# Performance work log

Hardware: AMD Instinct MI355X
Metric: run time of the kernel (lower is better)

## Reference

```python
import jax, jax.numpy as jnp
import numpy as np

V, E, H, L = 50257, 1024, 1024, 512


def setup_inputs() -> dict:
    key = jax.random.key(0)
    ks = jax.random.split(key, 12)
    s = 0.02
    return {
        'input': jax.random.randint(ks[0], (1,), 0, V),
        'hidden': jax.random.normal(ks[1], (1, 1, H), dtype=jnp.float32),
        'encoder_outputs': jax.random.normal(ks[2], (L, H), dtype=jnp.float32),
        'emb_table': jax.random.normal(ks[3], (V, E), dtype=jnp.float32) * s,
        'attn_W': jax.random.normal(ks[4], (L, E + H), dtype=jnp.float32) * s,
        'attn_b': jax.random.normal(ks[5], (L,), dtype=jnp.float32) * s,
        'W_ih': jax.random.normal(ks[6], (3 * H, E + H), dtype=jnp.float32) * s,
        'W_hh': jax.random.normal(ks[7], (3 * H, H), dtype=jnp.float32) * s,
        'b_ih': jax.random.normal(ks[8], (3 * H,), dtype=jnp.float32) * s,
        'b_hh': jax.random.normal(ks[9], (3 * H,), dtype=jnp.float32) * s,
        'out_W': jax.random.normal(ks[10], (V, H), dtype=jnp.float32) * s,
        'out_b': jax.random.normal(ks[11], (V,), dtype=jnp.float32) * s,
    }


def reference(input, hidden, encoder_outputs, emb_table, attn_W, attn_b,
              W_ih, W_hh, b_ih, b_hh, out_W, out_b):
    # Dropout is inference-identity here.
    embedded = emb_table[input].reshape(1, E)                      # [1, E]
    h = hidden[0]                                                  # [1, H]
    attn_in = jnp.concatenate([embedded, h], axis=1)               # [1, E+H]
    attn_weights = jax.nn.softmax(attn_in @ attn_W.T + attn_b, axis=1)  # [1, L]
    attn_applied = attn_weights @ encoder_outputs                  # [1, H]
    x = jnp.concatenate([embedded, attn_applied], axis=1)          # [1, E+H]
    # PyTorch GRU cell, gate order (r, z, n)
    gi = x @ W_ih.T + b_ih                                         # [1, 3H]
    gh = h @ W_hh.T + b_hh                                         # [1, 3H]
    i_r, i_z, i_n = gi[:, :H], gi[:, H:2 * H], gi[:, 2 * H:]
    h_r, h_z, h_n = gh[:, :H], gh[:, H:2 * H], gh[:, 2 * H:]
    r = jax.nn.sigmoid(i_r + h_r)
    z = jax.nn.sigmoid(i_z + h_z)
    n = jnp.tanh(i_n + r * h_n)
    h_new = (1.0 - z) * n + z * h                                  # [1, H]
    log_probs = jax.nn.log_softmax(h_new @ out_W.T + out_b, axis=1)  # [1, V]
    return log_probs, h_new[None], attn_weights
```

## Files before the change

kernel.cpp:

```cpp
#include <hip/hip_runtime.h>
#include <math.h>

#define V 50257
#define E 1024
#define H 1024
#define L 512

#define OUT_LP 0
#define OUT_H  50257
#define OUT_AW 51281

#define WS_S    0
#define WS_W    512
#define WS_X    1024
#define WS_GH   3072
#define WS_GI   6144
#define WS_HN   9216
#define WS_BMAX 10240
#define WS_SUM  12288
#define WS_MAX  12289

__global__ void k1_scores_gh(const int* __restrict__ input,
                             const float* __restrict__ hidden,
                             const float* __restrict__ emb_table,
                             const float* __restrict__ attn_W,
                             const float* __restrict__ attn_b,
                             const float* __restrict__ W_hh,
                             const float* __restrict__ b_hh,
                             float* __restrict__ ws) {
    int wave = (blockIdx.x * blockDim.x + threadIdx.x) >> 6;
    int lane = threadIdx.x & 63;
    const float4* h4 = (const float4*)hidden;
    if (wave < L) {
        int l = wave;
        const float4* emb4 = (const float4*)(emb_table + (size_t)input[0] * E);
        const float4* w4 = (const float4*)(attn_W + (size_t)l * (E + H));
        float acc = 0.f;
        for (int i = lane; i < (E + H) / 4; i += 64) {
            float4 a = (i < E / 4) ? emb4[i] : h4[i - E / 4];
            float4 b = w4[i];
            acc += a.x * b.x + a.y * b.y + a.z * b.z + a.w * b.w;
        }
        for (int off = 32; off > 0; off >>= 1) acc += __shfl_down(acc, off, 64);
        if (lane == 0) ws[WS_S + l] = acc + attn_b[l];
    } else {
        int k = wave - L;
        if (k < 3 * H) {
            const float4* w4 = (const float4*)(W_hh + (size_t)k * H);
            float acc = 0.f;
            for (int i = lane; i < H / 4; i += 64) {
                float4 a = h4[i];
                float4 b = w4[i];
                acc += a.x * b.x + a.y * b.y + a.z * b.z + a.w * b.w;
            }
            for (int off = 32; off > 0; off >>= 1) acc += __shfl_down(acc, off, 64);
            if (lane == 0) ws[WS_GH + k] = acc + b_hh[k];
        }
    }
}

__global__ void k2_softmax(const int* __restrict__ input,
                           const float* __restrict__ emb_table,
                           float* __restrict__ ws, float* __restrict__ out) {
    __shared__ float red[8];
    __shared__ float bmax, bsum;
    int t = threadIdx.x;
    int lane = t & 63, wid = t >> 6;
    float v = ws[WS_S + t];
    float m = v;
    for (int off = 32; off > 0; off >>= 1) m = fmaxf(m, __shfl_down(m, off, 64));
    if (lane == 0) red[wid] = m;
    __syncthreads();
    if (t == 0) {
        float mm = red[0];
        for (int i = 1; i < 8; i++) mm = fmaxf(mm, red[i]);
        bmax = mm;
    }
    __syncthreads();
    float e = expf(v - bmax);
    float s = e;
    for (int off = 32; off > 0; off >>= 1) s += __shfl_down(s, off, 64);
    if (lane == 0) red[wid] = s;
    __syncthreads();
    if (t == 0) {
        float ss = 0.f;
        for (int i = 0; i < 8; i++) ss += red[i];
        bsum = ss;
    }
    __syncthreads();
    float w = e / bsum;
    ws[WS_W + t] = w;
    out[OUT_AW + t] = w;
    const float* emb = emb_table + (size_t)input[0] * E;
    ws[WS_X + t] = emb[t];
    ws[WS_X + 512 + t] = emb[512 + t];
    ws[WS_X + E + t] = 0.f;
    ws[WS_X + E + 512 + t] = 0.f;
}

__global__ void k3_applied(const float* __restrict__ enc, float* __restrict__ ws) {
    int jc = blockIdx.x & 3, lc = blockIdx.x >> 2;
    int j = jc * 256 + threadIdx.x;
    int l0 = lc * 64;
    float acc = 0.f;
    for (int l = l0; l < l0 + 64; ++l)
        acc += ws[WS_W + l] * enc[(size_t)l * H + j];
    atomicAdd(&ws[WS_X + E + j], acc);
}

__global__ void k4_gi(const float* __restrict__ W_ih, const float* __restrict__ b_ih,
                      float* __restrict__ ws) {
    int wave = (blockIdx.x * blockDim.x + threadIdx.x) >> 6;
    int lane = threadIdx.x & 63;
    if (wave >= 3 * H) return;
    const float4* x4 = (const float4*)(ws + WS_X);
    const float4* w4 = (const float4*)(W_ih + (size_t)wave * (E + H));
    float acc = 0.f;
    for (int i = lane; i < (E + H) / 4; i += 64) {
        float4 a = x4[i];
        float4 b = w4[i];
        acc += a.x * b.x + a.y * b.y + a.z * b.z + a.w * b.w;
    }
    for (int off = 32; off > 0; off >>= 1) acc += __shfl_down(acc, off, 64);
    if (lane == 0) ws[WS_GI + wave] = acc + b_ih[wave];
}

__global__ void k5_combine(const float* __restrict__ hidden, float* __restrict__ ws,
                           float* __restrict__ out) {
    int k = blockIdx.x * 256 + threadIdx.x;
    float gir = ws[WS_GI + k],         ghr = ws[WS_GH + k];
    float giz = ws[WS_GI + H + k],     ghz = ws[WS_GH + H + k];
    float gin = ws[WS_GI + 2 * H + k], ghn = ws[WS_GH + 2 * H + k];
    float r = 1.f / (1.f + expf(-(gir + ghr)));
    float z = 1.f / (1.f + expf(-(giz + ghz)));
    float n = tanhf(gin + r * ghn);
    float hn = (1.f - z) * n + z * hidden[k];
    ws[WS_HN + k] = hn;
    out[OUT_H + k] = hn;
    if (k == 0) ws[WS_SUM] = 0.f;
}

__global__ void k6_logits(const float* __restrict__ out_W, const float* __restrict__ out_b,
                          float* __restrict__ ws, float* __restrict__ out) {
    __shared__ float hn[H];
    __shared__ float wmax[4];
    int t = threadIdx.x;
    for (int i = t; i < H; i += 256) hn[i] = ws[WS_HN + i];
    __syncthreads();
    int lane = t & 63, wid = t >> 6;
    int gwave = blockIdx.x * 4 + wid;
    float lmax = -INFINITY;
    const float4* h4 = (const float4*)hn;
    for (int row = gwave; row < V; row += 8192) {
        const float4* w4 = (const float4*)(out_W + (size_t)row * H);
        float acc = 0.f;
        for (int i = lane; i < H / 4; i += 64) {
            float4 a = h4[i];
            float4 b = w4[i];
            acc += a.x * b.x + a.y * b.y + a.z * b.z + a.w * b.w;
        }
        for (int off = 32; off > 0; off >>= 1) acc += __shfl_down(acc, off, 64);
        if (lane == 0) {
            float lg = acc + out_b[row];
            out[OUT_LP + row] = lg;
            lmax = fmaxf(lmax, lg);
        }
    }
    if (lane == 0) wmax[wid] = lmax;
    __syncthreads();
    if (t == 0) {
        float m = fmaxf(fmaxf(wmax[0], wmax[1]), fmaxf(wmax[2], wmax[3]));
        ws[WS_BMAX + blockIdx.x] = m;
    }
}

__global__ void k7_sumexp(float* __restrict__ ws, const float* __restrict__ out) {
    __shared__ float red[4];
    __shared__ float gmax;
    int t = threadIdx.x;
    int lane = t & 63, wid = t >> 6;
    float m = -INFINITY;
    for (int i = t; i < 2048; i += 256) m = fmaxf(m, ws[WS_BMAX + i]);
    for (int off = 32; off > 0; off >>= 1) m = fmaxf(m, __shfl_down(m, off, 64));
    if (lane == 0) red[wid] = m;
    __syncthreads();
    if (t == 0) gmax = fmaxf(fmaxf(red[0], red[1]), fmaxf(red[2], red[3]));
    __syncthreads();
    float M = gmax;
    float s = 0.f;
    for (int i = blockIdx.x * 256 + t; i < V; i += 64 * 256) s += expf(out[i] - M);
    for (int off = 32; off > 0; off >>= 1) s += __shfl_down(s, off, 64);
    if (lane == 0) red[wid] = s;
    __syncthreads();
    if (t == 0) {
        float bs = red[0] + red[1] + red[2] + red[3];
        atomicAdd(&ws[WS_SUM], bs);
        if (blockIdx.x == 0) ws[WS_MAX] = M;
    }
}

__global__ void k8_logprobs(const float* __restrict__ ws, float* __restrict__ out) {
    int i = blockIdx.x * 256 + threadIdx.x;
    if (i < V) out[i] = out[i] - ws[WS_MAX] - logf(ws[WS_SUM]);
}

extern "C" void kernel_launch(void* const* d_in, const int* in_sizes, int n_in,
                              void* d_out, int out_size, void* d_ws, size_t ws_size,
                              hipStream_t stream) {
    const int*   input   = (const int*)d_in[0];
    const float* hidden  = (const float*)d_in[1];
    const float* enc     = (const float*)d_in[2];
    const float* emb     = (const float*)d_in[3];
    const float* attn_W  = (const float*)d_in[4];
    const float* attn_b  = (const float*)d_in[5];
    const float* W_ih    = (const float*)d_in[6];
    const float* W_hh    = (const float*)d_in[7];
    const float* b_ih    = (const float*)d_in[8];
    const float* b_hh    = (const float*)d_in[9];
    const float* out_W   = (const float*)d_in[10];
    const float* out_b   = (const float*)d_in[11];
    float* out = (float*)d_out;
    float* ws  = (float*)d_ws;

    k1_scores_gh<<<896, 256, 0, stream>>>(input, hidden, emb, attn_W, attn_b, W_hh, b_hh, ws);
    k2_softmax<<<1, 512, 0, stream>>>(input, emb, ws, out);
    k3_applied<<<32, 256, 0, stream>>>(enc, ws);
    k4_gi<<<768, 256, 0, stream>>>(W_ih, b_ih, ws);
    k5_combine<<<4, 256, 0, stream>>>(hidden, ws, out);
    k6_logits<<<2048, 256, 0, stream>>>(out_W, out_b, ws, out);
    k7_sumexp<<<64, 256, 0, stream>>>(ws, out);
    k8_logprobs<<<197, 256, 0, stream>>>(ws, out);
}
```

Measured before the change: 451.1 us.

## Fuse all decoder stages into one cooperative megakernel with online log-softmax

Replaces the eight separate kernel launches with one cooperative kernel of 1024 blocks, with grid-wide syncs between the stages. The vocab-projection stage now keeps a running max and sum per wave (online softmax), so the separate pass that re-read the logits to compute sum-of-exp is gone. This is meant to remove launch gaps and one extra pass over the large output vector. In exchange it adds six grid barriers and halves the number of waves streaming out_W compared with the earlier 2048-block logits launch.

```diff
diff --git a/kernel.cpp b/kernel.cpp
--- a/kernel.cpp
+++ b/kernel.cpp
@@ -1,207 +1,204 @@
 #include <hip/hip_runtime.h>
+#include <hip/hip_cooperative_groups.h>
 #include <math.h>
+
+namespace cg = cooperative_groups;
 
 #define V 50257
 #define E 1024
 #define H 1024
 #define L 512
-
-#define OUT_LP 0
+#define NBLK 1024
+
 #define OUT_H  50257
 #define OUT_AW 51281
 
 #define WS_S    0
-#define WS_W    512
 #define WS_X    1024
 #define WS_GH   3072
 #define WS_GI   6144
 #define WS_HN   9216
-#define WS_BMAX 10240
-#define WS_SUM  12288
-#define WS_MAX  12289
-
-__global__ void k1_scores_gh(const int* __restrict__ input,
-                             const float* __restrict__ hidden,
-                             const float* __restrict__ emb_table,
-                             const float* __restrict__ attn_W,
-                             const float* __restrict__ attn_b,
-                             const float* __restrict__ W_hh,
-                             const float* __restrict__ b_hh,
-                             float* __restrict__ ws) {
-    int wave = (blockIdx.x * blockDim.x + threadIdx.x) >> 6;
-    int lane = threadIdx.x & 63;
+#define WS_BM   10240
+#define WS_BS   11264
+#define WS_OFF  12288
+
+__device__ __forceinline__ float dot4(const float4 a, const float4 b) {
+    return a.x * b.x + a.y * b.y + a.z * b.z + a.w * b.w;
+}
+
+__device__ __forceinline__ float wave_sum(float v) {
+    for (int off = 32; off > 0; off >>= 1) v += __shfl_down(v, off, 64);
+    return v;
+}
+
+__global__ __launch_bounds__(256, 4)
+void mega(const int* __restrict__ input,
+          const float* __restrict__ hidden,
+          const float* __restrict__ enc,
+          const float* __restrict__ emb_table,
+          const float* __restrict__ attn_W,
+          const float* __restrict__ attn_b,
+          const float* __restrict__ W_ih,
+          const float* __restrict__ W_hh,
+          const float* __restrict__ b_ih,
+          const float* __restrict__ b_hh,
+          const float* __restrict__ out_W,
+          const float* __restrict__ out_b,
+          float* __restrict__ out,
+          float* __restrict__ ws) {
+    cg::grid_group grid = cg::this_grid();
+    __shared__ float smem[1040];
+    const int t = threadIdx.x;
+    const int lane = t & 63;
+    const int wid = t >> 6;
+    const int gwave = blockIdx.x * 4 + wid;
     const float4* h4 = (const float4*)hidden;
-    if (wave < L) {
-        int l = wave;
-        const float4* emb4 = (const float4*)(emb_table + (size_t)input[0] * E);
-        const float4* w4 = (const float4*)(attn_W + (size_t)l * (E + H));
+    const float* embrow = emb_table + (size_t)input[0] * E;
+    const float4* emb4 = (const float4*)embrow;
+
+    if (gwave < L) {
+        const float4* w4 = (const float4*)(attn_W + (size_t)gwave * (E + H));
         float acc = 0.f;
         for (int i = lane; i < (E + H) / 4; i += 64) {
             float4 a = (i < E / 4) ? emb4[i] : h4[i - E / 4];
-            float4 b = w4[i];
-            acc += a.x * b.x + a.y * b.y + a.z * b.z + a.w * b.w;
-        }
-        for (int off = 32; off > 0; off >>= 1) acc += __shfl_down(acc, off, 64);
-        if (lane == 0) ws[WS_S + l] = acc + attn_b[l];
-    } else {
-        int k = wave - L;
-        if (k < 3 * H) {
-            const float4* w4 = (const float4*)(W_hh + (size_t)k * H);
+            acc += dot4(a, w4[i]);
+        }
+        acc = wave_sum(acc);
+        if (lane == 0) ws[WS_S + gwave] = acc + attn_b[gwave];
+    } else if (gwave < L + 3 * H) {
+        int k = gwave - L;
+        const float4* w4 = (const float4*)(W_hh + (size_t)k * H);
+        float acc = 0.f;
+        for (int i = lane; i < H / 4; i += 64) acc += dot4(h4[i], w4[i]);
+        acc = wave_sum(acc);
+        if (lane == 0) ws[WS_GH + k] = acc + b_hh[k];
+    } else if (gwave < 3600) {
+        ws[WS_X + E + (gwave - 3584) * 64 + lane] = 0.f;
+    } else if (gwave < 3616) {
+        int i = (gwave - 3600) * 64 + lane;
+        ws[WS_X + i] = embrow[i];
+    }
+    grid.sync();
+
+    if (blockIdx.x < 32) {
+        float v0 = ws[WS_S + t];
+        float v1 = ws[WS_S + t + 256];
+        float m = fmaxf(v0, v1);
+        for (int off = 32; off > 0; off >>= 1) m = fmaxf(m, __shfl_down(m, off, 64));
+        if (lane == 0) smem[512 + wid] = m;
+        __syncthreads();
+        if (t == 0)
+            smem[520] = fmaxf(fmaxf(smem[512], smem[513]), fmaxf(smem[514], smem[515]));
+        __syncthreads();
+        float bm = smem[520];
+        float e0 = expf(v0 - bm), e1 = expf(v1 - bm);
+        float s = wave_sum(e0 + e1);
+        if (lane == 0) smem[516 + wid] = s;
+        __syncthreads();
+        if (t == 0) smem[521] = smem[516] + smem[517] + smem[518] + smem[519];
+        __syncthreads();
+        float inv = 1.f / smem[521];
+        float w0 = e0 * inv, w1 = e1 * inv;
+        smem[t] = w0;
+        smem[t + 256] = w1;
+        if (blockIdx.x == 0) { out[OUT_AW + t] = w0; out[OUT_AW + t + 256] = w1; }
+        __syncthreads();
+        int jc = blockIdx.x & 3, lc = blockIdx.x >> 2;
+        int j = jc * 256 + t;
+        int l0 = lc * 64;
+        float acc = 0.f;
+        for (int l = l0; l < l0 + 64; ++l) acc += smem[l] * enc[(size_t)l * H + j];
+        atomicAdd(&ws[WS_X + E + j], acc);
+    }
+    grid.sync();
+
+    if (gwave < 3 * H) {
+        const float4* x4 = (const float4*)(ws + WS_X);
+        const float4* w4 = (const float4*)(W_ih + (size_t)gwave * (E + H));
+        float acc = 0.f;
+        for (int i = lane; i < (E + H) / 4; i += 64) acc += dot4(x4[i], w4[i]);
+        acc = wave_sum(acc);
+        if (lane == 0) ws[WS_GI + gwave] = acc + b_ih[gwave];
+    }
+    grid.sync();
+
+    if (blockIdx.x < 4) {
+        int k = blockIdx.x * 256 + t;
+        float gir = ws[WS_GI + k],         ghr = ws[WS_GH + k];
+        float giz = ws[WS_GI + H + k],     ghz = ws[WS_GH + H + k];
+        float gin = ws[WS_GI + 2 * H + k], ghn = ws[WS_GH + 2 * H + k];
+        float r = 1.f / (1.f + expf(-(gir + ghr)));
+        float z = 1.f / (1.f + expf(-(giz + ghz)));
+        float n = tanhf(gin + r * ghn);
+        float hn = (1.f - z) * n + z * hidden[k];
+        ws[WS_HN + k] = hn;
+        out[OUT_H + k] = hn;
+    }
+    grid.sync();
+
+    {
+        for (int i = t; i < H; i += 256) smem[i] = ws[WS_HN + i];
+        __syncthreads();
+        const float4* hn4 = (const float4*)smem;
+        float m = -INFINITY, s = 0.f;
+        for (int row = gwave; row < V; row += 4 * NBLK) {
+            const float4* w4 = (const float4*)(out_W + (size_t)row * H);
             float acc = 0.f;
-            for (int i = lane; i < H / 4; i += 64) {
-                float4 a = h4[i];
-                float4 b = w4[i];
-                acc += a.x * b.x + a.y * b.y + a.z * b.z + a.w * b.w;
+            for (int i = lane; i < H / 4; i += 64) acc += dot4(hn4[i], w4[i]);
+            acc = wave_sum(acc);
+            if (lane == 0) {
+                float lg = acc + out_b[row];
+                out[row] = lg;
+                if (lg > m) { s = s * expf(m - lg) + 1.f; m = lg; }
+                else        { s += expf(lg - m); }
             }
-            for (int off = 32; off > 0; off >>= 1) acc += __shfl_down(acc, off, 64);
-            if (lane == 0) ws[WS_GH + k] = acc + b_hh[k];
-        }
-    }
-}
-
-__global__ void k2_softmax(const int* __restrict__ input,
-                           const float* __restrict__ emb_table,
-                           float* __restrict__ ws, float* __restrict__ out) {
-    __shared__ float red[8];
-    __shared__ float bmax, bsum;
-    int t = threadIdx.x;
-    int lane = t & 63, wid = t >> 6;
-    float v = ws[WS_S + t];
-    float m = v;
-    for (int off = 32; off > 0; off >>= 1) m = fmaxf(m, __shfl_down(m, off, 64));
-    if (lane == 0) red[wid] = m;
-    __syncthreads();
-    if (t == 0) {
-        float mm = red[0];
-        for (int i = 1; i < 8; i++) mm = fmaxf(mm, red[i]);
-        bmax = mm;
-    }
-    __syncthreads();
-    float e = expf(v - bmax);
-    float s = e;
-    for (int off = 32; off > 0; off >>= 1) s += __shfl_down(s, off, 64);
-    if (lane == 0) red[wid] = s;
-    __syncthreads();
-    if (t == 0) {
-        float ss = 0.f;
-        for (int i = 0; i < 8; i++) ss += red[i];
-        bsum = ss;
-    }
-    __syncthreads();
-    float w = e / bsum;
-    ws[WS_W + t] = w;
-    out[OUT_AW + t] = w;
-    const float* emb = emb_table + (size_t)input[0] * E;
-    ws[WS_X + t] = emb[t];
-    ws[WS_X + 512 + t] = emb[512 + t];
-    ws[WS_X + E + t] = 0.f;
-    ws[WS_X + E + 512 + t] = 0.f;
-}
-
-__global__ void k3_applied(const float* __restrict__ enc, float* __restrict__ ws) {
-    int jc = blockIdx.x & 3, lc = blockIdx.x >> 2;
-    int j = jc * 256 + threadIdx.x;
-    int l0 = lc * 64;
-    float acc = 0.f;
-    for (int l = l0; l < l0 + 64; ++l)
-        acc += ws[WS_W + l] * enc[(size_t)l * H + j];
-    atomicAdd(&ws[WS_X + E + j], acc);
-}
-
-__global__ void k4_gi(const float* __restrict__ W_ih, const float* __restrict__ b_ih,
-                      float* __restrict__ ws) {
-    int wave = (blockIdx.x * blockDim.x + threadIdx.x) >> 6;
-    int lane = threadIdx.x & 63;
-    if (wave >= 3 * H) return;
-    const float4* x4 = (const float4*)(ws + WS_X);
-    const float4* w4 = (const float4*)(W_ih + (size_t)wave * (E + H));
-    float acc = 0.f;
-    for (int i = lane; i < (E + H) / 4; i += 64) {
-        float4 a = x4[i];
-        float4 b = w4[i];
-        acc += a.x * b.x + a.y * b.y + a.z * b.z + a.w * b.w;
-    }
-    for (int off = 32; off > 0; off >>= 1) acc += __shfl_down(acc, off, 64);
-    if (lane == 0) ws[WS_GI + wave] = acc + b_ih[wave];
-}
-
-__global__ void k5_combine(const float* __restrict__ hidden, float* __restrict__ ws,
-                           float* __restrict__ out) {
-    int k = blockIdx.x * 256 + threadIdx.x;
-    float gir = ws[WS_GI + k],         ghr = ws[WS_GH + k];
-    float giz = ws[WS_GI + H + k],     ghz = ws[WS_GH + H + k];
-    float gin = ws[WS_GI + 2 * H + k], ghn = ws[WS_GH + 2 * H + k];
-    float r = 1.f / (1.f + expf(-(gir + ghr)));
-    float z = 1.f / (1.f + expf(-(giz + ghz)));
-    float n = tanhf(gin + r * ghn);
-    float hn = (1.f - z) * n + z * hidden[k];
-    ws[WS_HN + k] = hn;
-    out[OUT_H + k] = hn;
-    if (k == 0) ws[WS_SUM] = 0.f;
-}
-
-__global__ void k6_logits(const float* __restrict__ out_W, const float* __restrict__ out_b,
-                          float* __restrict__ ws, float* __restrict__ out) {
-    __shared__ float hn[H];
-    __shared__ float wmax[4];
-    int t = threadIdx.x;
-    for (int i = t; i < H; i += 256) hn[i] = ws[WS_HN + i];
-    __syncthreads();
-    int lane = t & 63, wid = t >> 6;
-    int gwave = blockIdx.x * 4 + wid;
-    float lmax = -INFINITY;
-    const float4* h4 = (const float4*)hn;
-    for (int row = gwave; row < V; row += 8192) {
-        const float4* w4 = (const float4*)(out_W + (size_t)row * H);
-        float acc = 0.f;
-        for (int i = lane; i < H / 4; i += 64) {
-            float4 a = h4[i];
-            float4 b = w4[i];
-            acc += a.x * b.x + a.y * b.y + a.z * b.z + a.w * b.w;
-        }
-        for (int off = 32; off > 0; off >>= 1) acc += __shfl_down(acc, off, 64);
-        if (lane == 0) {
-            float lg = acc + out_b[row];
-            out[OUT_LP + row] = lg;
-            lmax = fmaxf(lmax, lg);
-        }
-    }
-    if (lane == 0) wmax[wid] = lmax;
-    __syncthreads();
-    if (t == 0) {
-        float m = fmaxf(fmaxf(wmax[0], wmax[1]), fmaxf(wmax[2], wmax[3]));
-        ws[WS_BMAX + blockIdx.x] = m;
-    }
-}
-
-__global__ void k7_sumexp(float* __restrict__ ws, const float* __restrict__ out) {
-    __shared__ float red[4];
-    __shared__ float gmax;
-    int t = threadIdx.x;
-    int lane = t & 63, wid = t >> 6;
-    float m = -INFINITY;
-    for (int i = t; i < 2048; i += 256) m = fmaxf(m, ws[WS_BMAX + i]);
-    for (int off = 32; off > 0; off >>= 1) m = fmaxf(m, __shfl_down(m, off, 64));
-    if (lane == 0) red[wid] = m;
-    __syncthreads();
-    if (t == 0) gmax = fmaxf(fmaxf(red[0], red[1]), fmaxf(red[2], red[3]));
-    __syncthreads();
-    float M = gmax;
-    float s = 0.f;
-    for (int i = blockIdx.x * 256 + t; i < V; i += 64 * 256) s += expf(out[i] - M);
-    for (int off = 32; off > 0; off >>= 1) s += __shfl_down(s, off, 64);
-    if (lane == 0) red[wid] = s;
-    __syncthreads();
-    if (t == 0) {
-        float bs = red[0] + red[1] + red[2] + red[3];
-        atomicAdd(&ws[WS_SUM], bs);
-        if (blockIdx.x == 0) ws[WS_MAX] = M;
-    }
-}
-
-__global__ void k8_logprobs(const float* __restrict__ ws, float* __restrict__ out) {
-    int i = blockIdx.x * 256 + threadIdx.x;
-    if (i < V) out[i] = out[i] - ws[WS_MAX] - logf(ws[WS_SUM]);
+        }
+        if (lane == 0) { smem[1024 + wid] = m; smem[1028 + wid] = s; }
+        __syncthreads();
+        if (t == 0) {
+            float M = fmaxf(fmaxf(smem[1024], smem[1025]), fmaxf(smem[1026], smem[1027]));
+            float S = smem[1028] * expf(smem[1024] - M) + smem[1029] * expf(smem[1025] - M)
+                    + smem[1030] * expf(smem[1026] - M) + smem[1031] * expf(smem[1027] - M);
+            ws[WS_BM + blockIdx.x] = M;
+            ws[WS_BS + blockIdx.x] = S;
+        }
+    }
+    grid.sync();
+
+    if (blockIdx.x == 0) {
+        float m = -INFINITY, s = 0.f;
+        for (int b = t; b < NBLK; b += 256) {
+            float bm = ws[WS_BM + b], bs = ws[WS_BS + b];
+            float M2 = fmaxf(m, bm);
+            s = s * expf(m - M2) + bs * expf(bm - M2);
+            m = M2;
+        }
+        for (int off = 32; off > 0; off >>= 1) {
+            float mo = __shfl_down(m, off, 64);
+            float so = __shfl_down(s, off, 64);
+            float M2 = fmaxf(m, mo);
+            s = s * expf(m - M2) + so * expf(mo - M2);
+            m = M2;
+        }
+        if (lane == 0) { smem[wid] = m; smem[4 + wid] = s; }
+        __syncthreads();
+        if (t == 0) {
+            float M = smem[0], S = smem[4];
+            for (int i = 1; i < 4; i++) {
+                float M2 = fmaxf(M, smem[i]);
+                S = S * expf(M - M2) + smem[4 + i] * expf(smem[i] - M2);
+                M = M2;
+            }
+            ws[WS_OFF] = M + logf(S);
+        }
+    }
+    grid.sync();
+
+    {
+        float off = ws[WS_OFF];
+        int i = blockIdx.x * 256 + t;
+        if (i < V) out[i] -= off;
+    }
 }
 
 extern "C" void kernel_launch(void* const* d_in, const int* in_sizes, int n_in,
@@ -222,12 +219,11 @@
     float* out = (float*)d_out;
     float* ws  = (float*)d_ws;
 
-    k1_scores_gh<<<896, 256, 0, stream>>>(input, hidden, emb, attn_W, attn_b, W_hh, b_hh, ws);
-    k2_softmax<<<1, 512, 0, stream>>>(input, emb, ws, out);
-    k3_applied<<<32, 256, 0, stream>>>(enc, ws);
-    k4_gi<<<768, 256, 0, stream>>>(W_ih, b_ih, ws);
-    k5_combine<<<4, 256, 0, stream>>>(hidden, ws, out);
-    k6_logits<<<2048, 256, 0, stream>>>(out_W, out_b, ws, out);
-    k7_sumexp<<<64, 256, 0, stream>>>(ws, out);
-    k8_logprobs<<<197, 256, 0, stream>>>(ws, out);
-}
+    void* args[] = {
+        (void*)&input, (void*)&hidden, (void*)&enc, (void*)&emb,
+        (void*)&attn_W, (void*)&attn_b, (void*)&W_ih, (void*)&W_hh,
+        (void*)&b_ih, (void*)&b_hh, (void*)&out_W, (void*)&out_b,
+        (void*)&out, (void*)&ws
+    };
+    hipLaunchCooperativeKernel((void*)mega, dim3(NBLK), dim3(256), args, 0, stream);
+}
```

Result: slower. 1.049 ms (+132.5%).
